# Kernel optimization log

Measured on AMD Instinct MI355X. Metric: run time of the kernel, lower is better.

Reference implementation:

```python
import jax, jax.numpy as jnp
import numpy as np

B, LQ, LD, H, DIM, PF = 16, 64, 2048, 1024, 128, 4
MAXK = LD // PF + 1  # static upper bound on num clusters (valid_len <= LD)


def setup_inputs() -> dict:
    key = jax.random.key(0)
    k1, k2, k3, k4 = jax.random.split(key, 4)
    return {
        "q_hidden": jax.random.normal(k1, (B, LQ, H), jnp.float32),
        "d_hidden": jax.random.normal(k2, (B, LD, H), jnp.float32),
        "W": jax.random.normal(k3, (H, DIM), jnp.float32) * (1.0 / np.sqrt(H)),  # xavier-ish
        "b": jnp.zeros((DIM,), jnp.float32),
        "q_mask": jnp.ones((B, LQ), jnp.int32),
        "d_mask": jnp.ones((B, LD), jnp.int32),
        "labels": jax.random.randint(k4, (B, LD), 0, MAXK, dtype=jnp.int32),
        "pooling_factor": PF,
    }


def _encode(hidden, W, b, mask):
    # proj -> L2 normalize -> zero out padded tokens
    r = hidden @ W + b
    r = r / jnp.clip(jnp.linalg.norm(r, axis=-1, keepdims=True), 1e-12)
    return r * mask[..., None].astype(r.dtype)


def _pool(d_repr, d_mask, labels, pf):
    # segment-mean per batch sample, cluster labels supplied externally
    Bn, L, D = d_repr.shape
    max_k = L // pf + 1  # static
    valid = jnp.clip(d_mask.sum(-1), 2, None)          # [B]
    k = valid // pf + 1                                 # per-sample num clusters
    lab = jnp.where(d_mask > 0, labels % k[:, None], max_k)  # invalid tokens -> dummy seg
    seg = lambda vals, idx: jax.ops.segment_sum(vals, idx, num_segments=max_k + 1)
    sums = jax.vmap(seg)(d_repr, lab)[:, :max_k]                          # [B,K,D]
    counts = jax.vmap(seg)(jnp.where(d_mask > 0, 1.0, 0.0), lab)[:, :max_k]
    means = sums / jnp.clip(counts, 1.0)[..., None]
    means = means / jnp.clip(jnp.linalg.norm(means, axis=-1, keepdims=True), 1e-12)
    pad_mask = jnp.arange(max_k)[None, :] < k[:, None]                    # [B,K]
    return means * pad_mask[..., None], pad_mask


def reference(q_hidden, d_hidden, W, b, q_mask, d_mask, labels, pooling_factor):
    q = _encode(q_hidden, W, b, q_mask)            # [B,LQ,DIM]
    d = _encode(d_hidden, W, b, d_mask)            # [B,LD,DIM]
    d_pool, pmask = _pool(d, d_mask, labels, pooling_factor)  # [B,K,DIM]
    sim = jnp.einsum('bqd,bkd->bqk', q, d_pool)
    sim = jnp.where(pmask[:, None, :], sim, -1e4)
    score = (sim.max(-1) * q_mask.astype(sim.dtype)).sum(-1)  # maxsum per pair
    return score
```

## Files before the change

### kernel.cpp

```cpp
#include <hip/hip_runtime.h>
#include <hip/hip_bf16.h>

#define BB    16
#define LQ    64
#define LD    2048
#define HH    1024
#define DIM   128
#define MAXK  513
#define SCH   9
#define NUNITS 2112
#define EGRID 512

typedef __attribute__((ext_vector_type(8))) short short8;
typedef __attribute__((ext_vector_type(4))) float f32x4;

__device__ __forceinline__ float b2f(ushort u) {
    union { float f; unsigned int u32; } c; c.u32 = ((unsigned int)u) << 16; return c.f;
}
__device__ __forceinline__ ushort f2b_rn(float f) {
    unsigned int x = __float_as_uint(f);
    return (ushort)((x + 0x7fffu + ((x >> 16) & 1u)) >> 16);
}

__device__ __forceinline__ void gld16(void* lds, const void* g) {
    __builtin_amdgcn_global_load_lds(
        (const __attribute__((address_space(1))) unsigned int*)g,
        (__attribute__((address_space(3))) unsigned int*)lds,
        16, 0, 0);
}

__global__ __launch_bounds__(256) void prep_kb_kernel(
    const float* __restrict__ W,
    const int*   __restrict__ d_mask,
    const int*   __restrict__ pf,
    ushort*      __restrict__ Wt,
    int*         __restrict__ kvals,
    float*       __restrict__ sums)
{
    int bid = blockIdx.x, t = threadIdx.x;
    if (bid < 16) {
        __shared__ ushort tile[128][72];
        const int h0 = bid * 64;
        #pragma unroll
        for (int i = 0; i < 32; ++i) {
            int flat = i * 256 + t;
            int r = flat >> 7, c = flat & 127;
            tile[c][r] = f2b_rn(W[(long)(h0 + r) * DIM + c]);
        }
        __syncthreads();
        #pragma unroll
        for (int i = 0; i < 4; ++i) {
            int flat = i * 256 + t;
            int n = flat >> 3, u = flat & 7;
            uint4 v = *(const uint4*)&tile[n][u * 8];
            *(uint4*)&Wt[(long)n * HH + h0 + u * 8] = v;
        }
    } else if (bid < 32) {
        __shared__ int red[4];
        int b = bid - 16;
        int lane = t & 63, wave = t >> 6;
        int s = 0;
        for (int i = t; i < LD; i += 256) s += (d_mask[b * LD + i] > 0) ? 1 : 0;
        #pragma unroll
        for (int m = 1; m < 64; m <<= 1) s += __shfl_xor(s, m);
        if (lane == 0) red[wave] = s;
        __syncthreads();
        if (t == 0) {
            int v = red[0] + red[1] + red[2] + red[3];
            if (v < 2) v = 2;
            int pfv = pf[0];
            if (pfv < 1 || pfv > LD) pfv = 4;
            kvals[b] = v / pfv + 1;
        }
    } else {
        const int total4 = (BB * MAXK * DIM) / 4;
        float4* s4 = (float4*)sums;
        const float4 z = make_float4(0.f, 0.f, 0.f, 0.f);
        for (int i = (bid - 32) * 256 + t; i < total4; i += 256 * 256)
            s4[i] = z;
    }
}

__global__ __launch_bounds__(512, 4) void encode_kernel(
    const float*  __restrict__ Xd,
    const float*  __restrict__ Xq,
    const ushort* __restrict__ Wt,
    const float*  __restrict__ bias,
    const int*    __restrict__ mask_d,
    const int*    __restrict__ mask_q,
    const int*    __restrict__ labels,
    const int*    __restrict__ kvals,
    float*        __restrict__ sums,
    float*        __restrict__ q_repr)
{
    __shared__ __align__(16) uint4 Wlds[4096];

    const int t = threadIdx.x;
    const int w = t >> 6, lane = t & 63;
    const int m16 = lane & 15, quad = lane >> 4;
    const int s = blockIdx.x * 8 + w;

    int unit = -1;
    if ((s & 1) == 0) unit = s >> 1;
    else if ((s & 63) == 1) unit = 2048 + (s >> 6);
    const bool active = unit >= 0;
    const bool isq = unit >= 2048;

    long row0 = 0;
    const float* aptr = Xd;
    if (active) {
        row0 = isq ? (long)(unit - 2048) * 16 : (long)unit * 16;
        const float* Xb = isq ? Xq : Xd;
        aptr = Xb + (row0 + m16) * HH + quad * 8;
    }

    f32x4 acc[8];
    #pragma unroll
    for (int j = 0; j < 8; ++j) acc[j] = (f32x4){0.f, 0.f, 0.f, 0.f};

    const int sw8 = m16 & 7;
    const ushort* Wu = (const ushort*)Wlds;

    float4 ast[3][2];
    if (active) {
        ast[0][0] = *(const float4*)(aptr);
        ast[0][1] = *(const float4*)(aptr + 4);
        ast[1][0] = *(const float4*)(aptr + 32);
        ast[1][1] = *(const float4*)(aptr + 32 + 4);
    }

    #pragma unroll
    for (int p = 0; p < 4; ++p) {
        __syncthreads();
        #pragma unroll
        for (int i = 0; i < 8; ++i) {
            int Si = w * 512 + i * 64 + lane;
            int n  = Si >> 5, up = Si & 31;
            const ushort* src = Wt + (long)n * HH + (p * 32 + (up ^ (n & 7))) * 8;
            gld16(&Wlds[w * 512 + i * 64], src);
        }
        __syncthreads();
        if (active) {
            #pragma unroll
            for (int cc = 0; cc < 8; ++cc) {
                const int c = p * 8 + cc;
                if (c + 2 < 32) {
                    ast[(c + 2) % 3][0] = *(const float4*)(aptr + (c + 2) * 32);
                    ast[(c + 2) % 3][1] = *(const float4*)(aptr + (c + 2) * 32 + 4);
                }
                float av[8];
                *(float4*)(av)     = ast[c % 3][0];
                *(float4*)(av + 4) = ast[c % 3][1];
                short8 ah, al;
                #pragma unroll
                for (int j = 0; j < 8; ++j) {
                    unsigned int ux = __float_as_uint(av[j]);
                    ah[j] = (short)(ux >> 16);
                    float hif = __uint_as_float(ux & 0xffff0000u);
                    al[j] = (short)(__float_as_uint(av[j] - hif) >> 16);
                }
                #pragma unroll
                for (int ct = 0; ct < 8; ++ct) {
                    short8 bf = *(const short8*)
                        &Wu[(ct * 16 + m16) * 256 + ((cc * 4 + quad) ^ sw8) * 8];
                    acc[ct] = __builtin_amdgcn_mfma_f32_16x16x32_bf16(ah, bf, acc[ct], 0, 0, 0);
                    acc[ct] = __builtin_amdgcn_mfma_f32_16x16x32_bf16(al, bf, acc[ct], 0, 0, 0);
                }
            }
        }
    }

    if (!active) return;

    float bia[8];
    #pragma unroll
    for (int ct = 0; ct < 8; ++ct) bia[ct] = bias[ct * 16 + m16];

    float vv[8][4];
    float ssp[4] = {0.f, 0.f, 0.f, 0.f};
    #pragma unroll
    for (int ct = 0; ct < 8; ++ct)
        #pragma unroll
        for (int r = 0; r < 4; ++r) {
            vv[ct][r] = acc[ct][r] + bia[ct];
            ssp[r] += vv[ct][r] * vv[ct][r];
        }
    #pragma unroll
    for (int r = 0; r < 4; ++r) {
        ssp[r] += __shfl_xor(ssp[r], 1);
        ssp[r] += __shfl_xor(ssp[r], 2);
        ssp[r] += __shfl_xor(ssp[r], 4);
        ssp[r] += __shfl_xor(ssp[r], 8);
    }

    #pragma unroll
    for (int r = 0; r < 4; ++r) {
        long rowg = row0 + quad * 4 + r;
        float scale = 1.0f / fmaxf(sqrtf(ssp[r]), 1e-12f);
        if (isq) {
            scale *= (float)mask_q[rowg];
            #pragma unroll
            for (int ct = 0; ct < 8; ++ct)
                q_repr[rowg * DIM + ct * 16 + m16] = vv[ct][r] * scale;
        } else if (mask_d[rowg] > 0) {
            int b = (int)(rowg >> 11);
            int seg = labels[rowg] % kvals[b];
            float* sp = sums + ((long)b * MAXK + seg) * DIM + m16;
            #pragma unroll
            for (int ct = 0; ct < 8; ++ct)
                atomicAdd(sp + ct * 16, vv[ct][r] * scale);
        }
    }
}

__global__ __launch_bounds__(256) void simmax_kernel(
    const float* __restrict__ q_repr,
    const float* __restrict__ sums,
    const int*   __restrict__ kvals,
    float*       __restrict__ pmax)
{
    __shared__ __align__(16) ushort Qh[64 * 136];
    __shared__ __align__(16) ushort Ql[64 * 136];
    __shared__ __align__(16) ushort Ch[64 * 136];
    __shared__ float cn[64];

    int b = blockIdx.x / SCH, chunk = blockIdx.x % SCH;
    int t = threadIdx.x, w = t >> 6, lane = t & 63;
    int m16 = lane & 15, quad = lane >> 4;

    #pragma unroll
    for (int i = 0; i < 8; ++i) {
        int flat = i * 256 + t;
        int row = flat >> 5, c4 = flat & 31;
        float4 v = *(const float4*)(q_repr + ((long)b * LQ + row) * DIM + c4 * 4);
        float x[4]; *(float4*)x = v;
        ushort4 h, l;
        ushort* hp = (ushort*)&h; ushort* lp = (ushort*)&l;
        #pragma unroll
        for (int j = 0; j < 4; ++j) {
            unsigned int ux = __float_as_uint(x[j]);
            hp[j] = (ushort)(ux >> 16);
            lp[j] = f2b_rn(x[j] - __uint_as_float(ux & 0xffff0000u));
        }
        *(ushort4*)&Qh[row * 136 + c4 * 4] = h;
        *(ushort4*)&Ql[row * 136 + c4 * 4] = l;
    }
    #pragma unroll
    for (int i = 0; i < 8; ++i) {
        int flat = i * 256 + t;
        int row = flat >> 5, c4 = flat & 31;
        int kk = chunk * 64 + row;
        float4 v = (kk < MAXK)
            ? *(const float4*)(sums + ((long)b * MAXK + kk) * DIM + c4 * 4)
            : make_float4(0.f, 0.f, 0.f, 0.f);
        ushort4 h; ushort* hp = (ushort*)&h;
        hp[0] = f2b_rn(v.x); hp[1] = f2b_rn(v.y);
        hp[2] = f2b_rn(v.z); hp[3] = f2b_rn(v.w);
        *(ushort4*)&Ch[row * 136 + c4 * 4] = h;
    }
    __syncthreads();

    {
        int c = w * 16 + m16;
        float ssv = 0.f;
        #pragma unroll
        for (int j = 0; j < 16; ++j) {
            unsigned int u = *(const unsigned int*)&Ch[c * 136 + quad * 32 + j * 2];
            float x0 = b2f((ushort)u), x1 = b2f((ushort)(u >> 16));
            ssv += x0 * x0 + x1 * x1;
        }
        ssv += __shfl_xor(ssv, 16);
        ssv += __shfl_xor(ssv, 32);
        if (quad == 0) cn[c] = (ssv > 1e-24f) ? rsqrtf(ssv) : 0.f;
    }
    __syncthreads();

    f32x4 acc[4];
    #pragma unroll
    for (int j = 0; j < 4; ++j) acc[j] = (f32x4){0.f, 0.f, 0.f, 0.f};

    #pragma unroll
    for (int kc = 0; kc < 4; ++kc) {
        short8 qh = *(const short8*)&Qh[(w * 16 + m16) * 136 + kc * 32 + quad * 8];
        short8 ql = *(const short8*)&Ql[(w * 16 + m16) * 136 + kc * 32 + quad * 8];
        #pragma unroll
        for (int ct = 0; ct < 4; ++ct) {
            short8 cf = *(const short8*)&Ch[(ct * 16 + m16) * 136 + kc * 32 + quad * 8];
            acc[ct] = __builtin_amdgcn_mfma_f32_16x16x32_bf16(qh, cf, acc[ct], 0, 0, 0);
            acc[ct] = __builtin_amdgcn_mfma_f32_16x16x32_bf16(ql, cf, acc[ct], 0, 0, 0);
        }
    }

    int kb = kvals[b];
    #pragma unroll
    for (int r = 0; r < 4; ++r) {
        float mx = -1e4f;
        #pragma unroll
        for (int ct = 0; ct < 4; ++ct) {
            int cl = chunk * 64 + ct * 16 + m16;
            float sim = acc[ct][r] * cn[ct * 16 + m16];
            mx = fmaxf(mx, (cl < kb) ? sim : -1e4f);
        }
        mx = fmaxf(mx, __shfl_xor(mx, 1));
        mx = fmaxf(mx, __shfl_xor(mx, 2));
        mx = fmaxf(mx, __shfl_xor(mx, 4));
        mx = fmaxf(mx, __shfl_xor(mx, 8));
        if (m16 == 0)
            pmax[((long)b * SCH + chunk) * 64 + w * 16 + quad * 4 + r] = mx;
    }
}

__global__ __launch_bounds__(64) void final_kernel(
    const float* __restrict__ pmax,
    const int*   __restrict__ q_mask,
    float*       __restrict__ out)
{
    int b = blockIdx.x, r = threadIdx.x;
    float m = -3e38f;
    #pragma unroll
    for (int c = 0; c < SCH; ++c)
        m = fmaxf(m, pmax[((long)b * SCH + c) * 64 + r]);
    m *= (float)q_mask[b * LQ + r];
    #pragma unroll
    for (int sh = 1; sh < 64; sh <<= 1) m += __shfl_xor(m, sh);
    if (r == 0) out[b] = m;
}

extern "C" void kernel_launch(void* const* d_in, const int* in_sizes, int n_in,
                              void* d_out, int out_size, void* d_ws, size_t ws_size,
                              hipStream_t stream) {
    const float* q_hidden = (const float*)d_in[0];
    const float* d_hidden = (const float*)d_in[1];
    const float* W        = (const float*)d_in[2];
    const float* bias     = (const float*)d_in[3];
    const int*   q_mask   = (const int*)d_in[4];
    const int*   d_mask   = (const int*)d_in[5];
    const int*   labels   = (const int*)d_in[6];
    const int*   pf       = (const int*)d_in[7];

    float* ws     = (float*)d_ws;
    float* q_repr = ws;
    float* sums   = q_repr + (long)BB * LQ * DIM;
    float* pmaxb  = sums + (long)BB * MAXK * DIM;
    int*   kvals  = (int*)(pmaxb + BB * SCH * 64);
    ushort* Wt    = (ushort*)(kvals + 16);

    prep_kb_kernel<<<288, 256, 0, stream>>>(W, d_mask, pf, Wt, kvals, sums);
    encode_kernel<<<EGRID, 512, 0, stream>>>(d_hidden, q_hidden, Wt, bias,
                                             d_mask, q_mask, labels, kvals,
                                             sums, q_repr);
    simmax_kernel<<<BB * SCH, 256, 0, stream>>>(q_repr, sums, kvals, pmaxb);
    final_kernel<<<BB, 64, 0, stream>>>(pmaxb, q_mask, (float*)d_out);
}
```

Before: 247.0 us.

## Fuse all stages into one cooperative persistent kernel with grid syncs

Replaces the four separate launches (prep, encode, simmax, final) with a single cooperative kernel of 132 blocks × 1024 threads that separates stages with grid-wide syncs. If the cooperative launch fails, it falls back to four staged launches. The encode stage now gives each wave a 16-row unit with no idle waves, and it deepens the A-prefetch ring from three to four slots. The simmax stage splits each 64-cluster chunk across 16 waves, each computing one 16x16 tile, which makes the partial-max buffer four times larger. The aim is to remove launch overhead and the idle half of the encode waves, at the cost of grid-sync latency and lower concurrency of blocks per CU.

```diff
diff --git a/kernel.cpp b/kernel.cpp
--- a/kernel.cpp
+++ b/kernel.cpp
@@ -1,5 +1,8 @@
 #include <hip/hip_runtime.h>
 #include <hip/hip_bf16.h>
+#include <hip/hip_cooperative_groups.h>
+
+namespace cg = cooperative_groups;
 
 #define BB    16
 #define LQ    64
@@ -8,8 +11,8 @@
 #define DIM   128
 #define MAXK  513
 #define SCH   9
-#define NUNITS 2112
-#define EGRID 512
+#define GRID  132
+#define NTH   1024
 
 typedef __attribute__((ext_vector_type(8))) short short8;
 typedef __attribute__((ext_vector_type(4))) float f32x4;
@@ -29,128 +32,126 @@
         16, 0, 0);
 }
 
-__global__ __launch_bounds__(256) void prep_kb_kernel(
-    const float* __restrict__ W,
-    const int*   __restrict__ d_mask,
-    const int*   __restrict__ pf,
-    ushort*      __restrict__ Wt,
-    int*         __restrict__ kvals,
-    float*       __restrict__ sums)
+union ShMem {
+    uint4  wbuf[4096];
+    ushort tile[128][72];
+    int    red[16];
+    struct {
+        ushort Qh[64 * 136];
+        ushort Ql[64 * 136];
+        ushort Ch[64 * 136];
+        float  cn[64];
+    } sm;
+};
+
+__global__ __launch_bounds__(NTH, 4) void fused_kernel(
+    const float*  __restrict__ Xq,
+    const float*  __restrict__ Xd,
+    const float*  __restrict__ W,
+    const float*  __restrict__ bias,
+    const int*    __restrict__ q_mask,
+    const int*    __restrict__ d_mask,
+    const int*    __restrict__ labels,
+    const int*    __restrict__ pf,
+    float*        __restrict__ q_repr,
+    float*        __restrict__ sums,
+    float*        __restrict__ pmax,
+    int*          __restrict__ kvals,
+    ushort*       __restrict__ Wt,
+    float*        __restrict__ out,
+    int           stage)
 {
-    int bid = blockIdx.x, t = threadIdx.x;
-    if (bid < 16) {
-        __shared__ ushort tile[128][72];
-        const int h0 = bid * 64;
-        #pragma unroll
-        for (int i = 0; i < 32; ++i) {
-            int flat = i * 256 + t;
-            int r = flat >> 7, c = flat & 127;
-            tile[c][r] = f2b_rn(W[(long)(h0 + r) * DIM + c]);
-        }
-        __syncthreads();
-        #pragma unroll
-        for (int i = 0; i < 4; ++i) {
-            int flat = i * 256 + t;
-            int n = flat >> 3, u = flat & 7;
-            uint4 v = *(const uint4*)&tile[n][u * 8];
-            *(uint4*)&Wt[(long)n * HH + h0 + u * 8] = v;
-        }
-    } else if (bid < 32) {
-        __shared__ int red[4];
-        int b = bid - 16;
-        int lane = t & 63, wave = t >> 6;
-        int s = 0;
-        for (int i = t; i < LD; i += 256) s += (d_mask[b * LD + i] > 0) ? 1 : 0;
-        #pragma unroll
-        for (int m = 1; m < 64; m <<= 1) s += __shfl_xor(s, m);
-        if (lane == 0) red[wave] = s;
-        __syncthreads();
-        if (t == 0) {
-            int v = red[0] + red[1] + red[2] + red[3];
-            if (v < 2) v = 2;
-            int pfv = pf[0];
-            if (pfv < 1 || pfv > LD) pfv = 4;
-            kvals[b] = v / pfv + 1;
-        }
-    } else {
-        const int total4 = (BB * MAXK * DIM) / 4;
-        float4* s4 = (float4*)sums;
-        const float4 z = make_float4(0.f, 0.f, 0.f, 0.f);
-        for (int i = (bid - 32) * 256 + t; i < total4; i += 256 * 256)
-            s4[i] = z;
-    }
-}
-
-__global__ __launch_bounds__(512, 4) void encode_kernel(
-    const float*  __restrict__ Xd,
-    const float*  __restrict__ Xq,
-    const ushort* __restrict__ Wt,
-    const float*  __restrict__ bias,
-    const int*    __restrict__ mask_d,
-    const int*    __restrict__ mask_q,
-    const int*    __restrict__ labels,
-    const int*    __restrict__ kvals,
-    float*        __restrict__ sums,
-    float*        __restrict__ q_repr)
-{
-    __shared__ __align__(16) uint4 Wlds[4096];
-
-    const int t = threadIdx.x;
+    __shared__ ShMem sh;
+    const int bid = blockIdx.x, t = threadIdx.x;
     const int w = t >> 6, lane = t & 63;
     const int m16 = lane & 15, quad = lane >> 4;
-    const int s = blockIdx.x * 8 + w;
-
-    int unit = -1;
-    if ((s & 1) == 0) unit = s >> 1;
-    else if ((s & 63) == 1) unit = 2048 + (s >> 6);
-    const bool active = unit >= 0;
-    const bool isq = unit >= 2048;
-
-    long row0 = 0;
-    const float* aptr = Xd;
-    if (active) {
-        row0 = isq ? (long)(unit - 2048) * 16 : (long)unit * 16;
+    const bool all = (stage < 0);
+
+    if (all || stage == 0) {
+        if (bid < 16) {
+            const int h0 = bid * 64;
+            #pragma unroll
+            for (int i = 0; i < 8; ++i) {
+                int flat = i * NTH + t;
+                int r = flat >> 7, c = flat & 127;
+                sh.tile[c][r] = f2b_rn(W[(h0 + r) * DIM + c]);
+            }
+            __syncthreads();
+            {
+                int n = t >> 3, uu = t & 7;
+                uint4 v = *(const uint4*)&sh.tile[n][uu * 8];
+                *(uint4*)&Wt[(long)n * HH + h0 + uu * 8] = v;
+            }
+        } else if (bid < 32) {
+            int b = bid - 16;
+            int s = 0;
+            for (int i = t; i < LD; i += NTH) s += (d_mask[b * LD + i] > 0) ? 1 : 0;
+            #pragma unroll
+            for (int m = 1; m < 64; m <<= 1) s += __shfl_xor(s, m);
+            if (lane == 0) sh.red[w] = s;
+            __syncthreads();
+            if (t == 0) {
+                int v = 0;
+                #pragma unroll
+                for (int i = 0; i < 16; ++i) v += sh.red[i];
+                if (v < 2) v = 2;
+                int pfv = pf[0];
+                if (pfv < 1 || pfv > LD) pfv = 4;
+                kvals[b] = v / pfv + 1;
+            }
+        } else {
+            const int total4 = (BB * MAXK * DIM) / 4;
+            float4* s4 = (float4*)sums;
+            const float4 z = make_float4(0.f, 0.f, 0.f, 0.f);
+            for (int i = (bid - 32) * NTH + t; i < total4; i += 100 * NTH)
+                s4[i] = z;
+        }
+    }
+    if (all) { __syncthreads(); __threadfence(); cg::this_grid().sync(); }
+
+    if (all || stage == 1) {
+        const int unit = bid * 16 + w;
+        const bool isq = unit >= 2048;
+        const long row0 = isq ? (long)(unit - 2048) * 16 : (long)unit * 16;
         const float* Xb = isq ? Xq : Xd;
-        aptr = Xb + (row0 + m16) * HH + quad * 8;
-    }
-
-    f32x4 acc[8];
-    #pragma unroll
-    for (int j = 0; j < 8; ++j) acc[j] = (f32x4){0.f, 0.f, 0.f, 0.f};
-
-    const int sw8 = m16 & 7;
-    const ushort* Wu = (const ushort*)Wlds;
-
-    float4 ast[3][2];
-    if (active) {
+        const float* aptr = Xb + (row0 + m16) * HH + quad * 8;
+
+        f32x4 acc[8];
+        #pragma unroll
+        for (int j = 0; j < 8; ++j) acc[j] = (f32x4){0.f, 0.f, 0.f, 0.f};
+
+        const int sw8 = m16 & 7;
+        const ushort* Wu = (const ushort*)sh.wbuf;
+
+        float4 ast[4][2];
         ast[0][0] = *(const float4*)(aptr);
         ast[0][1] = *(const float4*)(aptr + 4);
         ast[1][0] = *(const float4*)(aptr + 32);
-        ast[1][1] = *(const float4*)(aptr + 32 + 4);
-    }
-
-    #pragma unroll
-    for (int p = 0; p < 4; ++p) {
-        __syncthreads();
-        #pragma unroll
-        for (int i = 0; i < 8; ++i) {
-            int Si = w * 512 + i * 64 + lane;
-            int n  = Si >> 5, up = Si & 31;
-            const ushort* src = Wt + (long)n * HH + (p * 32 + (up ^ (n & 7))) * 8;
-            gld16(&Wlds[w * 512 + i * 64], src);
-        }
-        __syncthreads();
-        if (active) {
+        ast[1][1] = *(const float4*)(aptr + 36);
+        ast[2][0] = *(const float4*)(aptr + 64);
+        ast[2][1] = *(const float4*)(aptr + 68);
+
+        #pragma unroll
+        for (int p = 0; p < 4; ++p) {
+            __syncthreads();
+            #pragma unroll
+            for (int i = 0; i < 4; ++i) {
+                int Si = w * 256 + i * 64 + lane;
+                int n = Si >> 5, up = Si & 31;
+                const ushort* src = Wt + (long)n * HH + (p * 32 + (up ^ (n & 7))) * 8;
+                gld16(&sh.wbuf[w * 256 + i * 64], src);
+            }
+            __syncthreads();
             #pragma unroll
             for (int cc = 0; cc < 8; ++cc) {
                 const int c = p * 8 + cc;
-                if (c + 2 < 32) {
-                    ast[(c + 2) % 3][0] = *(const float4*)(aptr + (c + 2) * 32);
-                    ast[(c + 2) % 3][1] = *(const float4*)(aptr + (c + 2) * 32 + 4);
+                if (c + 3 < 32) {
+                    ast[(c + 3) & 3][0] = *(const float4*)(aptr + (c + 3) * 32);
+                    ast[(c + 3) & 3][1] = *(const float4*)(aptr + (c + 3) * 32 + 4);
                 }
                 float av[8];
-                *(float4*)(av)     = ast[c % 3][0];
-                *(float4*)(av + 4) = ast[c % 3][1];
+                *(float4*)(av)     = ast[c & 3][0];
+                *(float4*)(av + 4) = ast[c & 3][1];
                 short8 ah, al;
                 #pragma unroll
                 for (int j = 0; j < 8; ++j) {
@@ -168,162 +169,141 @@
                 }
             }
         }
-    }
-
-    if (!active) return;
-
-    float bia[8];
-    #pragma unroll
-    for (int ct = 0; ct < 8; ++ct) bia[ct] = bias[ct * 16 + m16];
-
-    float vv[8][4];
-    float ssp[4] = {0.f, 0.f, 0.f, 0.f};
-    #pragma unroll
-    for (int ct = 0; ct < 8; ++ct)
+
+        float bia[8];
+        #pragma unroll
+        for (int ct = 0; ct < 8; ++ct) bia[ct] = bias[ct * 16 + m16];
+
+        float vv[8][4];
+        float ssp[4] = {0.f, 0.f, 0.f, 0.f};
+        #pragma unroll
+        for (int ct = 0; ct < 8; ++ct)
+            #pragma unroll
+            for (int r = 0; r < 4; ++r) {
+                vv[ct][r] = acc[ct][r] + bia[ct];
+                ssp[r] += vv[ct][r] * vv[ct][r];
+            }
         #pragma unroll
         for (int r = 0; r < 4; ++r) {
-            vv[ct][r] = acc[ct][r] + bia[ct];
-            ssp[r] += vv[ct][r] * vv[ct][r];
-        }
-    #pragma unroll
-    for (int r = 0; r < 4; ++r) {
-        ssp[r] += __shfl_xor(ssp[r], 1);
-        ssp[r] += __shfl_xor(ssp[r], 2);
-        ssp[r] += __shfl_xor(ssp[r], 4);
-        ssp[r] += __shfl_xor(ssp[r], 8);
-    }
-
-    #pragma unroll
-    for (int r = 0; r < 4; ++r) {
-        long rowg = row0 + quad * 4 + r;
-        float scale = 1.0f / fmaxf(sqrtf(ssp[r]), 1e-12f);
-        if (isq) {
-            scale *= (float)mask_q[rowg];
-            #pragma unroll
-            for (int ct = 0; ct < 8; ++ct)
-                q_repr[rowg * DIM + ct * 16 + m16] = vv[ct][r] * scale;
-        } else if (mask_d[rowg] > 0) {
-            int b = (int)(rowg >> 11);
-            int seg = labels[rowg] % kvals[b];
-            float* sp = sums + ((long)b * MAXK + seg) * DIM + m16;
-            #pragma unroll
-            for (int ct = 0; ct < 8; ++ct)
-                atomicAdd(sp + ct * 16, vv[ct][r] * scale);
-        }
-    }
-}
-
-__global__ __launch_bounds__(256) void simmax_kernel(
-    const float* __restrict__ q_repr,
-    const float* __restrict__ sums,
-    const int*   __restrict__ kvals,
-    float*       __restrict__ pmax)
-{
-    __shared__ __align__(16) ushort Qh[64 * 136];
-    __shared__ __align__(16) ushort Ql[64 * 136];
-    __shared__ __align__(16) ushort Ch[64 * 136];
-    __shared__ float cn[64];
-
-    int b = blockIdx.x / SCH, chunk = blockIdx.x % SCH;
-    int t = threadIdx.x, w = t >> 6, lane = t & 63;
-    int m16 = lane & 15, quad = lane >> 4;
-
-    #pragma unroll
-    for (int i = 0; i < 8; ++i) {
-        int flat = i * 256 + t;
-        int row = flat >> 5, c4 = flat & 31;
-        float4 v = *(const float4*)(q_repr + ((long)b * LQ + row) * DIM + c4 * 4);
-        float x[4]; *(float4*)x = v;
-        ushort4 h, l;
-        ushort* hp = (ushort*)&h; ushort* lp = (ushort*)&l;
-        #pragma unroll
-        for (int j = 0; j < 4; ++j) {
-            unsigned int ux = __float_as_uint(x[j]);
-            hp[j] = (ushort)(ux >> 16);
-            lp[j] = f2b_rn(x[j] - __uint_as_float(ux & 0xffff0000u));
-        }
-        *(ushort4*)&Qh[row * 136 + c4 * 4] = h;
-        *(ushort4*)&Ql[row * 136 + c4 * 4] = l;
-    }
-    #pragma unroll
-    for (int i = 0; i < 8; ++i) {
-        int flat = i * 256 + t;
-        int row = flat >> 5, c4 = flat & 31;
-        int kk = chunk * 64 + row;
-        float4 v = (kk < MAXK)
-            ? *(const float4*)(sums + ((long)b * MAXK + kk) * DIM + c4 * 4)
-            : make_float4(0.f, 0.f, 0.f, 0.f);
-        ushort4 h; ushort* hp = (ushort*)&h;
-        hp[0] = f2b_rn(v.x); hp[1] = f2b_rn(v.y);
-        hp[2] = f2b_rn(v.z); hp[3] = f2b_rn(v.w);
-        *(ushort4*)&Ch[row * 136 + c4 * 4] = h;
-    }
-    __syncthreads();
-
-    {
-        int c = w * 16 + m16;
-        float ssv = 0.f;
-        #pragma unroll
-        for (int j = 0; j < 16; ++j) {
-            unsigned int u = *(const unsigned int*)&Ch[c * 136 + quad * 32 + j * 2];
-            float x0 = b2f((ushort)u), x1 = b2f((ushort)(u >> 16));
-            ssv += x0 * x0 + x1 * x1;
-        }
-        ssv += __shfl_xor(ssv, 16);
-        ssv += __shfl_xor(ssv, 32);
-        if (quad == 0) cn[c] = (ssv > 1e-24f) ? rsqrtf(ssv) : 0.f;
-    }
-    __syncthreads();
-
-    f32x4 acc[4];
-    #pragma unroll
-    for (int j = 0; j < 4; ++j) acc[j] = (f32x4){0.f, 0.f, 0.f, 0.f};
-
-    #pragma unroll
-    for (int kc = 0; kc < 4; ++kc) {
-        short8 qh = *(const short8*)&Qh[(w * 16 + m16) * 136 + kc * 32 + quad * 8];
-        short8 ql = *(const short8*)&Ql[(w * 16 + m16) * 136 + kc * 32 + quad * 8];
-        #pragma unroll
-        for (int ct = 0; ct < 4; ++ct) {
-            short8 cf = *(const short8*)&Ch[(ct * 16 + m16) * 136 + kc * 32 + quad * 8];
-            acc[ct] = __builtin_amdgcn_mfma_f32_16x16x32_bf16(qh, cf, acc[ct], 0, 0, 0);
-            acc[ct] = __builtin_amdgcn_mfma_f32_16x16x32_bf16(ql, cf, acc[ct], 0, 0, 0);
-        }
-    }
-
-    int kb = kvals[b];
-    #pragma unroll
-    for (int r = 0; r < 4; ++r) {
-        float mx = -1e4f;
-        #pragma unroll
-        for (int ct = 0; ct < 4; ++ct) {
-            int cl = chunk * 64 + ct * 16 + m16;
-            float sim = acc[ct][r] * cn[ct * 16 + m16];
-            mx = fmaxf(mx, (cl < kb) ? sim : -1e4f);
-        }
-        mx = fmaxf(mx, __shfl_xor(mx, 1));
-        mx = fmaxf(mx, __shfl_xor(mx, 2));
-        mx = fmaxf(mx, __shfl_xor(mx, 4));
-        mx = fmaxf(mx, __shfl_xor(mx, 8));
-        if (m16 == 0)
-            pmax[((long)b * SCH + chunk) * 64 + w * 16 + quad * 4 + r] = mx;
-    }
-}
-
-__global__ __launch_bounds__(64) void final_kernel(
-    const float* __restrict__ pmax,
-    const int*   __restrict__ q_mask,
-    float*       __restrict__ out)
-{
-    int b = blockIdx.x, r = threadIdx.x;
-    float m = -3e38f;
-    #pragma unroll
-    for (int c = 0; c < SCH; ++c)
-        m = fmaxf(m, pmax[((long)b * SCH + c) * 64 + r]);
-    m *= (float)q_mask[b * LQ + r];
-    #pragma unroll
-    for (int sh = 1; sh < 64; sh <<= 1) m += __shfl_xor(m, sh);
-    if (r == 0) out[b] = m;
+            ssp[r] += __shfl_xor(ssp[r], 1);
+            ssp[r] += __shfl_xor(ssp[r], 2);
+            ssp[r] += __shfl_xor(ssp[r], 4);
+            ssp[r] += __shfl_xor(ssp[r], 8);
+        }
+
+        #pragma unroll
+        for (int r = 0; r < 4; ++r) {
+            long rowg = row0 + quad * 4 + r;
+            float scale = 1.0f / fmaxf(sqrtf(ssp[r]), 1e-12f);
+            if (isq) {
+                scale *= (float)q_mask[rowg];
+                #pragma unroll
+                for (int ct = 0; ct < 8; ++ct)
+                    q_repr[rowg * DIM + ct * 16 + m16] = vv[ct][r] * scale;
+            } else if (d_mask[rowg] > 0) {
+                int b = (int)(rowg >> 11);
+                int seg = labels[rowg] % kvals[b];
+                float* sp = sums + ((long)b * MAXK + seg) * DIM + m16;
+                #pragma unroll
+                for (int ct = 0; ct < 8; ++ct)
+                    atomicAdd(sp + ct * 16, vv[ct][r] * scale);
+            }
+        }
+    }
+    if (all) { __threadfence(); cg::this_grid().sync(); }
+
+    if (all || stage == 2) {
+        for (int item = bid; item < BB * SCH; item += GRID) {
+            __syncthreads();
+            const int b = item & 15, ch = item >> 4;
+
+            #pragma unroll
+            for (int i = 0; i < 2; ++i) {
+                int flat = i * NTH + t;
+                int row = flat >> 5, c4 = flat & 31;
+                float4 v = *(const float4*)(q_repr + ((long)b * LQ + row) * DIM + c4 * 4);
+                float x[4]; *(float4*)x = v;
+                ushort4 h, l;
+                ushort* hp = (ushort*)&h; ushort* lp = (ushort*)&l;
+                #pragma unroll
+                for (int j = 0; j < 4; ++j) {
+                    unsigned int ux = __float_as_uint(x[j]);
+                    hp[j] = (ushort)(ux >> 16);
+                    lp[j] = f2b_rn(x[j] - __uint_as_float(ux & 0xffff0000u));
+                }
+                *(ushort4*)&sh.sm.Qh[row * 136 + c4 * 4] = h;
+                *(ushort4*)&sh.sm.Ql[row * 136 + c4 * 4] = l;
+            }
+            #pragma unroll
+            for (int i = 0; i < 2; ++i) {
+                int flat = i * NTH + t;
+                int row = flat >> 5, c4 = flat & 31;
+                int kk = ch * 64 + row;
+                float4 v = (kk < MAXK)
+                    ? *(const float4*)(sums + ((long)b * MAXK + kk) * DIM + c4 * 4)
+                    : make_float4(0.f, 0.f, 0.f, 0.f);
+                ushort4 h; ushort* hp = (ushort*)&h;
+                hp[0] = f2b_rn(v.x); hp[1] = f2b_rn(v.y);
+                hp[2] = f2b_rn(v.z); hp[3] = f2b_rn(v.w);
+                *(ushort4*)&sh.sm.Ch[row * 136 + c4 * 4] = h;
+            }
+            __syncthreads();
+
+            if (t < 256) {
+                int c = t >> 2, q4 = t & 3;
+                float ssv = 0.f;
+                #pragma unroll
+                for (int j = 0; j < 16; ++j) {
+                    unsigned int u = *(const unsigned int*)&sh.sm.Ch[c * 136 + q4 * 32 + j * 2];
+                    float x0 = b2f((ushort)u), x1 = b2f((ushort)(u >> 16));
+                    ssv += x0 * x0 + x1 * x1;
+                }
+                ssv += __shfl_xor(ssv, 1);
+                ssv += __shfl_xor(ssv, 2);
+                if (q4 == 0) sh.sm.cn[c] = (ssv > 1e-24f) ? rsqrtf(ssv) : 0.f;
+            }
+            __syncthreads();
+
+            const int qb = (w & 3) * 16, cb = (w >> 2) * 16;
+            f32x4 a2 = (f32x4){0.f, 0.f, 0.f, 0.f};
+            #pragma unroll
+            for (int kc = 0; kc < 4; ++kc) {
+                short8 qh = *(const short8*)&sh.sm.Qh[(qb + m16) * 136 + kc * 32 + quad * 8];
+                short8 ql = *(const short8*)&sh.sm.Ql[(qb + m16) * 136 + kc * 32 + quad * 8];
+                short8 cf = *(const short8*)&sh.sm.Ch[(cb + m16) * 136 + kc * 32 + quad * 8];
+                a2 = __builtin_amdgcn_mfma_f32_16x16x32_bf16(qh, cf, a2, 0, 0, 0);
+                a2 = __builtin_amdgcn_mfma_f32_16x16x32_bf16(ql, cf, a2, 0, 0, 0);
+            }
+            int kb = kvals[b];
+            #pragma unroll
+            for (int r = 0; r < 4; ++r) {
+                int cll = cb + m16;
+                int cl = ch * 64 + cll;
+                float sim = a2[r] * sh.sm.cn[cll];
+                float mx = (cl < kb) ? sim : -1e4f;
+                mx = fmaxf(mx, __shfl_xor(mx, 1));
+                mx = fmaxf(mx, __shfl_xor(mx, 2));
+                mx = fmaxf(mx, __shfl_xor(mx, 4));
+                mx = fmaxf(mx, __shfl_xor(mx, 8));
+                if (m16 == 0)
+                    pmax[(((long)b * SCH + ch) * 4 + (w >> 2)) * 64 + qb + quad * 4 + r] = mx;
+            }
+        }
+    }
+    if (all) { __threadfence(); cg::this_grid().sync(); }
+
+    if (all || stage == 3) {
+        if (bid < BB && t < 64) {
+            float m = -3e38f;
+            #pragma unroll
+            for (int s2 = 0; s2 < SCH * 4; ++s2)
+                m = fmaxf(m, pmax[(long)bid * (SCH * 4 * 64) + s2 * 64 + t]);
+            m *= (float)q_mask[bid * LQ + t];
+            #pragma unroll
+            for (int sh2 = 1; sh2 < 64; sh2 <<= 1) m += __shfl_xor(m, sh2);
+            if (t == 0) out[bid] = m;
+        }
+    }
 }
 
 extern "C" void kernel_launch(void* const* d_in, const int* in_sizes, int n_in,
@@ -342,13 +322,22 @@
     float* q_repr = ws;
     float* sums   = q_repr + (long)BB * LQ * DIM;
     float* pmaxb  = sums + (long)BB * MAXK * DIM;
-    int*   kvals  = (int*)(pmaxb + BB * SCH * 64);
+    int*   kvals  = (int*)(pmaxb + (long)BB * SCH * 4 * 64);
     ushort* Wt    = (ushort*)(kvals + 16);
-
-    prep_kb_kernel<<<288, 256, 0, stream>>>(W, d_mask, pf, Wt, kvals, sums);
-    encode_kernel<<<EGRID, 512, 0, stream>>>(d_hidden, q_hidden, Wt, bias,
-                                             d_mask, q_mask, labels, kvals,
-                                             sums, q_repr);
-    simmax_kernel<<<BB * SCH, 256, 0, stream>>>(q_repr, sums, kvals, pmaxb);
-    final_kernel<<<BB, 64, 0, stream>>>(pmaxb, q_mask, (float*)d_out);
-}
+    float* outp   = (float*)d_out;
+
+    int stage_all = -1;
+    void* args[] = { (void*)&q_hidden, (void*)&d_hidden, (void*)&W, (void*)&bias,
+                     (void*)&q_mask, (void*)&d_mask, (void*)&labels, (void*)&pf,
+                     (void*)&q_repr, (void*)&sums, (void*)&pmaxb, (void*)&kvals,
+                     (void*)&Wt, (void*)&outp, (void*)&stage_all };
+    hipError_t err = hipLaunchCooperativeKernel((const void*)fused_kernel,
+                                                dim3(GRID), dim3(NTH),
+                                                args, 0, stream);
+    if (err != hipSuccess) {
+        for (int s = 0; s < 4; ++s)
+            fused_kernel<<<GRID, NTH, 0, stream>>>(
+                q_hidden, d_hidden, W, bias, q_mask, d_mask, labels, pf,
+                q_repr, sums, pmaxb, kvals, Wt, outp, s);
+    }
+}
```

After: 416.2 us. 68.5% more time.

## Drop split-bf16 low part, split encode into dense q/d launches

Applied to the files above, without the earlier changes.

Converts the fp32 activations to a single round-to-nearest bf16 value instead of a hi+lo split, which halves the MFMA count in the projection GEMM. The encode kernel is split into two launches, one for queries and one for documents, so every wave does useful work; previously half of the waves in a 512-block grid sat idle. The activation prefetch depth also grows from 2 to 3 chunks. The trade-off is lower GEMM precision, since activations now carry only bf16 mantissa bits, which may move results outside the reference tolerance.

```diff
diff --git a/kernel.cpp b/kernel.cpp
--- a/kernel.cpp
+++ b/kernel.cpp
@@ -8,8 +8,6 @@
 #define DIM   128
 #define MAXK  513
 #define SCH   9
-#define NUNITS 2112
-#define EGRID 512
 
 typedef __attribute__((ext_vector_type(8))) short short8;
 typedef __attribute__((ext_vector_type(4))) float f32x4;
@@ -82,37 +80,25 @@
 }
 
 __global__ __launch_bounds__(512, 4) void encode_kernel(
-    const float*  __restrict__ Xd,
-    const float*  __restrict__ Xq,
+    const float*  __restrict__ X,
     const ushort* __restrict__ Wt,
     const float*  __restrict__ bias,
-    const int*    __restrict__ mask_d,
-    const int*    __restrict__ mask_q,
+    const int*    __restrict__ mask,
     const int*    __restrict__ labels,
     const int*    __restrict__ kvals,
     float*        __restrict__ sums,
-    float*        __restrict__ q_repr)
+    float*        __restrict__ q_repr,
+    int           isq)
 {
     __shared__ __align__(16) uint4 Wlds[4096];
 
     const int t = threadIdx.x;
     const int w = t >> 6, lane = t & 63;
     const int m16 = lane & 15, quad = lane >> 4;
-    const int s = blockIdx.x * 8 + w;
-
-    int unit = -1;
-    if ((s & 1) == 0) unit = s >> 1;
-    else if ((s & 63) == 1) unit = 2048 + (s >> 6);
-    const bool active = unit >= 0;
-    const bool isq = unit >= 2048;
-
-    long row0 = 0;
-    const float* aptr = Xd;
-    if (active) {
-        row0 = isq ? (long)(unit - 2048) * 16 : (long)unit * 16;
-        const float* Xb = isq ? Xq : Xd;
-        aptr = Xb + (row0 + m16) * HH + quad * 8;
-    }
+
+    const int unit = blockIdx.x * 8 + w;
+    const long row0 = (long)unit * 16;
+    const float* aptr = X + (row0 + m16) * HH + quad * 8;
 
     f32x4 acc[8];
     #pragma unroll
@@ -121,13 +107,13 @@
     const int sw8 = m16 & 7;
     const ushort* Wu = (const ushort*)Wlds;
 
-    float4 ast[3][2];
-    if (active) {
-        ast[0][0] = *(const float4*)(aptr);
-        ast[0][1] = *(const float4*)(aptr + 4);
-        ast[1][0] = *(const float4*)(aptr + 32);
-        ast[1][1] = *(const float4*)(aptr + 32 + 4);
-    }
+    float4 ast[4][2];
+    ast[0][0] = *(const float4*)(aptr);
+    ast[0][1] = *(const float4*)(aptr + 4);
+    ast[1][0] = *(const float4*)(aptr + 32);
+    ast[1][1] = *(const float4*)(aptr + 36);
+    ast[2][0] = *(const float4*)(aptr + 64);
+    ast[2][1] = *(const float4*)(aptr + 68);
 
     #pragma unroll
     for (int p = 0; p < 4; ++p) {
@@ -135,42 +121,32 @@
         #pragma unroll
         for (int i = 0; i < 8; ++i) {
             int Si = w * 512 + i * 64 + lane;
-            int n  = Si >> 5, up = Si & 31;
+            int n = Si >> 5, up = Si & 31;
             const ushort* src = Wt + (long)n * HH + (p * 32 + (up ^ (n & 7))) * 8;
             gld16(&Wlds[w * 512 + i * 64], src);
         }
         __syncthreads();
-        if (active) {
+        #pragma unroll
+        for (int cc = 0; cc < 8; ++cc) {
+            const int c = p * 8 + cc;
+            if (c + 3 < 32) {
+                ast[(c + 3) & 3][0] = *(const float4*)(aptr + (c + 3) * 32);
+                ast[(c + 3) & 3][1] = *(const float4*)(aptr + (c + 3) * 32 + 4);
+            }
+            float av[8];
+            *(float4*)(av)     = ast[c & 3][0];
+            *(float4*)(av + 4) = ast[c & 3][1];
+            short8 ah;
             #pragma unroll
-            for (int cc = 0; cc < 8; ++cc) {
-                const int c = p * 8 + cc;
-                if (c + 2 < 32) {
-                    ast[(c + 2) % 3][0] = *(const float4*)(aptr + (c + 2) * 32);
-                    ast[(c + 2) % 3][1] = *(const float4*)(aptr + (c + 2) * 32 + 4);
-                }
-                float av[8];
-                *(float4*)(av)     = ast[c % 3][0];
-                *(float4*)(av + 4) = ast[c % 3][1];
-                short8 ah, al;
-                #pragma unroll
-                for (int j = 0; j < 8; ++j) {
-                    unsigned int ux = __float_as_uint(av[j]);
-                    ah[j] = (short)(ux >> 16);
-                    float hif = __uint_as_float(ux & 0xffff0000u);
-                    al[j] = (short)(__float_as_uint(av[j] - hif) >> 16);
-                }
-                #pragma unroll
-                for (int ct = 0; ct < 8; ++ct) {
-                    short8 bf = *(const short8*)
-                        &Wu[(ct * 16 + m16) * 256 + ((cc * 4 + quad) ^ sw8) * 8];
-                    acc[ct] = __builtin_amdgcn_mfma_f32_16x16x32_bf16(ah, bf, acc[ct], 0, 0, 0);
-                    acc[ct] = __builtin_amdgcn_mfma_f32_16x16x32_bf16(al, bf, acc[ct], 0, 0, 0);
-                }
+            for (int j = 0; j < 8; ++j) ah[j] = (short)f2b_rn(av[j]);
+            #pragma unroll
+            for (int ct = 0; ct < 8; ++ct) {
+                short8 bf = *(const short8*)
+                    &Wu[(ct * 16 + m16) * 256 + ((cc * 4 + quad) ^ sw8) * 8];
+                acc[ct] = __builtin_amdgcn_mfma_f32_16x16x32_bf16(ah, bf, acc[ct], 0, 0, 0);
             }
         }
     }
-
-    if (!active) return;
 
     float bia[8];
     #pragma unroll
@@ -198,11 +174,11 @@
         long rowg = row0 + quad * 4 + r;
         float scale = 1.0f / fmaxf(sqrtf(ssp[r]), 1e-12f);
         if (isq) {
-            scale *= (float)mask_q[rowg];
+            scale *= (float)mask[rowg];
             #pragma unroll
             for (int ct = 0; ct < 8; ++ct)
                 q_repr[rowg * DIM + ct * 16 + m16] = vv[ct][r] * scale;
-        } else if (mask_d[rowg] > 0) {
+        } else if (mask[rowg] > 0) {
             int b = (int)(rowg >> 11);
             int seg = labels[rowg] % kvals[b];
             float* sp = sums + ((long)b * MAXK + seg) * DIM + m16;
@@ -346,9 +322,10 @@
     ushort* Wt    = (ushort*)(kvals + 16);
 
     prep_kb_kernel<<<288, 256, 0, stream>>>(W, d_mask, pf, Wt, kvals, sums);
-    encode_kernel<<<EGRID, 512, 0, stream>>>(d_hidden, q_hidden, Wt, bias,
-                                             d_mask, q_mask, labels, kvals,
-                                             sums, q_repr);
+    encode_kernel<<<8, 512, 0, stream>>>(q_hidden, Wt, bias, q_mask,
+                                         labels, kvals, sums, q_repr, 1);
+    encode_kernel<<<256, 512, 0, stream>>>(d_hidden, Wt, bias, d_mask,
+                                           labels, kvals, sums, q_repr, 0);
     simmax_kernel<<<BB * SCH, 256, 0, stream>>>(q_repr, sums, kvals, pmaxb);
     final_kernel<<<BB, 64, 0, stream>>>(pmaxb, q_mask, (float*)d_out);
 }
```

New measurement: 280.3 us. 13.5% more time.
